# Kernel tuning notes

Measured on AMD Instinct MI355X. Metric: run time of the kernel, lower is better.

## Reference

```python
import jax, jax.numpy as jnp
import numpy as np

N_NODES = 100000
N_EDGES = 1600000
IN_DIM = 256
OUT_DIM = 128


def setup_inputs() -> dict:
    key = jax.random.key(0)
    k1, k2, k3, k4, k5 = jax.random.split(key, 5)
    x = jax.random.normal(k1, (N_NODES, IN_DIM), dtype=jnp.float32)
    W = jax.random.normal(k2, (OUT_DIM, IN_DIM), dtype=jnp.float32) * (1.0 / np.sqrt(IN_DIM))
    edge_row = jax.random.randint(k3, (N_EDGES,), 0, N_NODES, dtype=jnp.int32)
    edge_col = jax.random.randint(k4, (N_EDGES,), 0, N_NODES, dtype=jnp.int32)
    # normalized adjacency values (positive, like D^-1/2 A D^-1/2 entries)
    edge_val = jax.random.uniform(k5, (N_EDGES,), dtype=jnp.float32)
    return {"x": x, "W": W, "edge_row": edge_row, "edge_col": edge_col, "edge_val": edge_val}


def reference(x, W, edge_row, edge_col, edge_val):
    # h = x @ W.T  (Linear without bias), shape [N, out_dim]
    h = jnp.einsum('ni,oi->no', x, W)
    # SpMM: out[r] = sum_{e: row[e]==r} val[e] * h[col[e]]
    msgs = h[edge_col] * edge_val[:, None]           # [E, out_dim] irregular gather
    out = jax.ops.segment_sum(msgs, edge_row, num_segments=x.shape[0])
    return out
```

## Files before the change

kernel.cpp:

```cpp
#include <hip/hip_runtime.h>
#include <hip/hip_fp16.h>

#define N_NODES 100000
#define N_EDGES 1600000
#define IN_DIM  256
#define OUT_DIM 128

#define BROWS  256
#define NBKT   391
#define CAP    4608
#define CHUNK  8192
#define NBLK   196
#define DCAP   6144

#define BMT    32
#define NTILE  (N_NODES / BMT)
#define TPB    4
#define NGBLK  ((NTILE + TPB - 1) / TPB)

typedef __attribute__((ext_vector_type(8))) short short8;
typedef __attribute__((ext_vector_type(4))) float f32x4;
typedef __attribute__((ext_vector_type(2))) float f32x2;

__device__ __forceinline__ unsigned short f2bf(float f) {
    unsigned int u = __float_as_uint(f);
    u += 0x7FFFu + ((u >> 16) & 1u);
    return (unsigned short)(u >> 16);
}
__device__ __forceinline__ float bf2f(unsigned int u16) {
    return __uint_as_float(u16 << 16);
}

__device__ __forceinline__ short8 pack8(float4 a, float4 b) {
    short8 s;
    s[0] = (short)f2bf(a.x); s[1] = (short)f2bf(a.y);
    s[2] = (short)f2bf(a.z); s[3] = (short)f2bf(a.w);
    s[4] = (short)f2bf(b.x); s[5] = (short)f2bf(b.y);
    s[6] = (short)f2bf(b.z); s[7] = (short)f2bf(b.w);
    return s;
}

__global__ __launch_bounds__(256) void w_to_bf16(const float* __restrict__ W,
                                                 unsigned short* __restrict__ Wb,
                                                 int* __restrict__ bcnt) {
    int i = blockIdx.x * 256 + threadIdx.x;
    if (i < OUT_DIM * IN_DIM) Wb[i] = f2bf(W[i]);
    if (blockIdx.x == 0) {
        for (int b = threadIdx.x; b < NBKT; b += 256) bcnt[b] = 0;
    }
}

__global__ __launch_bounds__(512) void gemm_bin(const float* __restrict__ x,
                                                const unsigned short* __restrict__ Wb,
                                                unsigned short* __restrict__ hb,
                                                const int* __restrict__ erow,
                                                const int* __restrict__ ecol,
                                                const float* __restrict__ eval,
                                                int* __restrict__ bcnt,
                                                int2* __restrict__ gbuf) {
    __shared__ unsigned short xs[2 * BMT * 256];
    const int tid = threadIdx.x;

    if (blockIdx.x < NBLK) {
        int* h    = (int*)xs;
        int* gpos = h + NBKT;
        int* rcur = gpos + NBKT;
        for (int i = tid; i < NBKT; i += 512) { h[i] = 0; rcur[i] = 0; }
        __syncthreads();
        const int e0 = blockIdx.x * CHUNK;
        for (int i = tid; i < CHUNK; i += 512) {
            int e = e0 + i;
            if (e < N_EDGES) atomicAdd(&h[erow[e] >> 8], 1);
        }
        __syncthreads();
        for (int i = tid; i < NBKT; i += 512)
            gpos[i] = h[i] ? (i * CAP + atomicAdd(&bcnt[i], h[i])) : 0;
        __syncthreads();
        for (int i = tid; i < CHUNK; i += 512) {
            int e = e0 + i;
            if (e < N_EDGES) {
                int r = erow[e];
                int b = r >> 8;
                unsigned int vb  = __half_as_ushort(__float2half(eval[e]));
                unsigned int rec = (vb << 17) | (unsigned int)ecol[e];
                int pos = gpos[b] + atomicAdd(&rcur[b], 1);
                gbuf[pos] = make_int2((int)rec, r);
            }
        }
        return;
    }

    const int g    = blockIdx.x - NBLK;
    const int t0   = g * TPB;
    const int wid  = tid >> 6;
    const int lane = tid & 63;
    const int l15  = lane & 15;
    const int g8   = (lane >> 4) * 8;
    const int col  = wid * 16 + l15;
    const int sw   = (l15 & 7) << 4;
    char* lb = (char*)xs;

    const int srow = tid >> 4;
    const int ca   = (tid & 15) * 8;
    const int swr  = (srow & 7) << 4;
    const int wbA  = (srow * 512 + ca * 2) ^ swr;
    const int wbB  = (srow * 512 + (ca + 128) * 2) ^ swr;

    short8 bfr[8];
    const unsigned short* wrow = Wb + (size_t)col * IN_DIM + g8;
#pragma unroll
    for (int kk = 0; kk < 8; ++kk)
        bfr[kk] = *(const short8*)(wrow + kk * 32);

    {
        const int ti = t0;
        const int gr = (ti < NTILE) ? (ti * BMT + srow) : srow;
        const float4* sA = (const float4*)(x + (size_t)gr * IN_DIM + ca);
        const float4* sB = (const float4*)(x + (size_t)gr * IN_DIM + ca + 128);
        float4 f0 = sA[0], f1 = sA[1], f2 = sB[0], f3 = sB[1];
        *(short8*)(lb + wbA) = pack8(f0, f1);
        *(short8*)(lb + wbB) = pack8(f2, f3);
    }

#pragma unroll
    for (int i = 0; i < TPB; ++i) {
        float4 q0, q1, q2, q3;
        if (i + 1 < TPB) {
            const int ti = t0 + i + 1;
            const int gr = (ti < NTILE) ? (ti * BMT + srow) : srow;
            const float4* sA = (const float4*)(x + (size_t)gr * IN_DIM + ca);
            const float4* sB = (const float4*)(x + (size_t)gr * IN_DIM + ca + 128);
            q0 = sA[0]; q1 = sA[1]; q2 = sB[0]; q3 = sB[1];
        }
        __syncthreads();

        const int ti = t0 + i;
        const char* cb = lb + (i & 1) * (BMT * 512);
        short8 a0[8], a1[8];
#pragma unroll
        for (int kk = 0; kk < 8; ++kk) {
            a0[kk] = *(const short8*)(cb + ((l15 * 512 + (kk * 32 + g8) * 2) ^ sw));
            a1[kk] = *(const short8*)(cb + (((l15 + 16) * 512 + (kk * 32 + g8) * 2) ^ sw));
        }
        f32x4 acc0 = {0.f, 0.f, 0.f, 0.f}, acc1 = {0.f, 0.f, 0.f, 0.f};
#pragma unroll
        for (int kk = 0; kk < 8; ++kk) {
            acc0 = __builtin_amdgcn_mfma_f32_16x16x32_bf16(a0[kk], bfr[kk], acc0, 0, 0, 0);
            acc1 = __builtin_amdgcn_mfma_f32_16x16x32_bf16(a1[kk], bfr[kk], acc1, 0, 0, 0);
        }
        if (ti < NTILE) {
            const int rb0 = ti * BMT + (lane >> 4) * 4;
            const int rb1 = rb0 + 16;
#pragma unroll
            for (int q = 0; q < 4; ++q) {
                hb[(size_t)(rb0 + q) * OUT_DIM + col] = f2bf(acc0[q]);
                hb[(size_t)(rb1 + q) * OUT_DIM + col] = f2bf(acc1[q]);
            }
        }

        if (i + 1 < TPB) {
            char* wbuf = lb + ((i + 1) & 1) * (BMT * 512);
            *(short8*)(wbuf + wbA) = pack8(q0, q1);
            *(short8*)(wbuf + wbB) = pack8(q2, q3);
        }
    }
}

__global__ __launch_bounds__(256) void sort_bucket(const int2* __restrict__ gbuf,
                                                   const int* __restrict__ bcnt,
                                                   unsigned int* __restrict__ gcsr,
                                                   int* __restrict__ offs,
                                                   int* __restrict__ bend) {
    __shared__ int rh[BROWS], rc[BROWS], tmp[256];
    __shared__ unsigned int lout[DCAP];
    const int b    = blockIdx.x;
    const int base = b * CAP;
    const int cnt  = bcnt[b];
    const int r0   = b * BROWS;
    const int t    = threadIdx.x;

    rh[t] = 0;
    __syncthreads();
    for (int i = t; i < cnt; i += 256)
        atomicAdd(&rh[gbuf[base + i].y - r0], 1);
    __syncthreads();

    int v = rh[t];
    tmp[t] = v;
    __syncthreads();
    for (int d = 1; d < 256; d <<= 1) {
        int a = (t >= d) ? tmp[t - d] : 0;
        __syncthreads();
        tmp[t] += a;
        __syncthreads();
    }
    int ex = tmp[t] - v;
    rc[t] = ex;
    offs[r0 + t] = base + ex;
    if (t == 0) bend[b] = base + cnt;
    __syncthreads();

    if (cnt <= DCAP) {
        for (int i = t; i < cnt; i += 256) {
            int2 rr = gbuf[base + i];
            int p = atomicAdd(&rc[rr.y - r0], 1);
            lout[p] = (unsigned int)rr.x;
        }
        __syncthreads();
        for (int i = t; i < cnt; i += 256)
            gcsr[base + i] = lout[i];
    } else {
        for (int i = t; i < cnt; i += 256) {
            int2 rr = gbuf[base + i];
            int p = atomicAdd(&rc[rr.y - r0], 1);
            gcsr[base + p] = (unsigned int)rr.x;
        }
    }
}

__global__ __launch_bounds__(256) void spmm_gather(const unsigned short* __restrict__ hb,
                                                   const int* __restrict__ offs,
                                                   const int* __restrict__ bend,
                                                   const unsigned int* __restrict__ ccv,
                                                   float* __restrict__ out) {
    const int lane = threadIdx.x & 63;
    const int half = lane >> 5;
    const int li   = lane & 31;
    const int r    = blockIdx.x * 8 + (threadIdx.x >> 6) * 2 + half;

    const int js = offs[r];
    const int je = ((r & (BROWS - 1)) == (BROWS - 1)) ? bend[r >> 8] : offs[r + 1];

    f32x2 accA = {0.f, 0.f}, accB = {0.f, 0.f};
    for (int j = js; __any(j < je); j += 8) {
        unsigned int e[8];
        uint2 p[8];
#pragma unroll
        for (int q = 0; q < 8; ++q) {
            int jj = j + q;
            e[q] = ccv[jj < je ? jj : 0];
        }
#pragma unroll
        for (int q = 0; q < 8; ++q)
            p[q] = *(const uint2*)(hb + (size_t)(e[q] & 0x1FFFFu) * OUT_DIM + li * 4);
#pragma unroll
        for (int q = 0; q < 8; ++q) {
            float v = (j + q < je)
                    ? __half2float(__ushort_as_half((unsigned short)(e[q] >> 17)))
                    : 0.f;
            f32x2 vv  = {v, v};
            f32x2 h01 = { __uint_as_float(p[q].x << 16),
                          __uint_as_float(p[q].x & 0xFFFF0000u) };
            f32x2 h23 = { __uint_as_float(p[q].y << 16),
                          __uint_as_float(p[q].y & 0xFFFF0000u) };
            accA = __builtin_elementwise_fma(vv, h01, accA);
            accB = __builtin_elementwise_fma(vv, h23, accB);
        }
    }
    float4 o = {accA.x, accA.y, accB.x, accB.y};
    *(float4*)(out + (size_t)r * OUT_DIM + li * 4) = o;
}

__global__ __launch_bounds__(512) void gemm_plain(const float* __restrict__ x,
                                                  const float* __restrict__ W,
                                                  unsigned short* __restrict__ hb) {
    __shared__ unsigned short xs[2 * BMT * 256];
    const int tid = threadIdx.x;
    const int m0  = blockIdx.x * (2 * BMT);
    char* lb = (char*)xs;
    {
        const int row = tid >> 3;
        const int cs  = (tid & 7) * 32;
        const int gr  = m0 + row;
        if (gr < N_NODES) {
            const float4* src = (const float4*)(x + (size_t)gr * IN_DIM + cs);
#pragma unroll
            for (int i = 0; i < 4; ++i) {
                float4 a = src[2 * i], b = src[2 * i + 1];
                int byt = (row * 512 + (cs + 8 * i) * 2) ^ ((row & 7) << 4);
                *(short8*)(lb + byt) = pack8(a, b);
            }
        } else {
            short8 z = {0, 0, 0, 0, 0, 0, 0, 0};
#pragma unroll
            for (int i = 0; i < 4; ++i) {
                int byt = (row * 512 + (cs + 8 * i) * 2) ^ ((row & 7) << 4);
                *(short8*)(lb + byt) = z;
            }
        }
    }
    __syncthreads();
    const int wid  = tid >> 6;
    const int lane = tid & 63;
    const int l15  = lane & 15;
    const int g8   = (lane >> 4) * 8;
    short8 bfr[8];
    const float* wrowf = W + (size_t)(wid * 16 + l15) * IN_DIM + g8;
#pragma unroll
    for (int kk = 0; kk < 8; ++kk) {
        float4 wa = *(const float4*)(wrowf + kk * 32);
        float4 wb = *(const float4*)(wrowf + kk * 32 + 4);
        bfr[kk] = pack8(wa, wb);
    }
    const int col = wid * 16 + l15;
    const int sw  = (l15 & 7) << 4;
    const char* lbc = (const char*)xs;
#pragma unroll
    for (int rp = 0; rp < 2; ++rp) {
        const int r0 = rp * 32 + l15;
        const int r1 = r0 + 16;
        short8 a0[8], a1[8];
#pragma unroll
        for (int kk = 0; kk < 8; ++kk) {
            a0[kk] = *(const short8*)(lbc + ((r0 * 512 + (kk * 32 + g8) * 2) ^ sw));
            a1[kk] = *(const short8*)(lbc + ((r1 * 512 + (kk * 32 + g8) * 2) ^ sw));
        }
        f32x4 acc0 = {0.f, 0.f, 0.f, 0.f}, acc1 = {0.f, 0.f, 0.f, 0.f};
#pragma unroll
        for (int kk = 0; kk < 8; ++kk) {
            acc0 = __builtin_amdgcn_mfma_f32_16x16x32_bf16(a0[kk], bfr[kk], acc0, 0, 0, 0);
            acc1 = __builtin_amdgcn_mfma_f32_16x16x32_bf16(a1[kk], bfr[kk], acc1, 0, 0, 0);
        }
        const int rb0 = m0 + rp * 32 + (lane >> 4) * 4;
        const int rb1 = rb0 + 16;
#pragma unroll
        for (int i = 0; i < 4; ++i) {
            if (rb0 + i < N_NODES) hb[(size_t)(rb0 + i) * OUT_DIM + col] = f2bf(acc0[i]);
            if (rb1 + i < N_NODES) hb[(size_t)(rb1 + i) * OUT_DIM + col] = f2bf(acc1[i]);
        }
    }
}

__global__ __launch_bounds__(256) void spmm_scatter(const unsigned short* __restrict__ hb,
                                                    const int* __restrict__ erow,
                                                    const int* __restrict__ ecol,
                                                    const float* __restrict__ eval,
                                                    float* __restrict__ out) {
    const int lane = threadIdx.x & 63;
    const int eloc = threadIdx.x >> 6;
    const int stride = gridDim.x * 4;
    for (int e = blockIdx.x * 4 + eloc; e < N_EDGES; e += stride) {
        const int r = erow[e];
        const int c = ecol[e];
        const float v = eval[e];
        unsigned int p = *(const unsigned int*)(hb + (size_t)c * OUT_DIM + lane * 2);
        float* o = out + (size_t)r * OUT_DIM + lane * 2;
        unsafeAtomicAdd(o + 0, v * bf2f(p & 0xFFFFu));
        unsafeAtomicAdd(o + 1, v * bf2f(p >> 16));
    }
}

extern "C" void kernel_launch(void* const* d_in, const int* in_sizes, int n_in,
                              void* d_out, int out_size, void* d_ws, size_t ws_size,
                              hipStream_t stream) {
    const float* x    = (const float*)d_in[0];
    const float* W    = (const float*)d_in[1];
    const int*   erow = (const int*)d_in[2];
    const int*   ecol = (const int*)d_in[3];
    const float* eval = (const float*)d_in[4];
    float*       out  = (float*)d_out;

    const size_t H_ELEMS = (size_t)N_NODES * OUT_DIM;
    unsigned short* hb    = (unsigned short*)d_ws;
    int2*           gbuf  = (int2*)(hb + H_ELEMS);
    unsigned int*   gcsr  = (unsigned int*)(gbuf + (size_t)NBKT * CAP);
    int*            offs  = (int*)(gcsr + (size_t)NBKT * CAP);
    int*            bend  = offs + NBKT * BROWS + 8;
    int*            bcnt  = bend + NBKT;
    unsigned short* Wb    = (unsigned short*)(bcnt + NBKT + 8);
    const size_t need = ((char*)(Wb + OUT_DIM * IN_DIM)) - (char*)d_ws;

    if (ws_size >= need) {
        w_to_bf16<<<(OUT_DIM * IN_DIM + 255) / 256, 256, 0, stream>>>(W, Wb, bcnt);
        gemm_bin<<<NBLK + NGBLK, 512, 0, stream>>>(x, Wb, hb, erow, ecol, eval, bcnt, gbuf);
        sort_bucket<<<NBKT, 256, 0, stream>>>(gbuf, bcnt, gcsr, offs, bend);
        spmm_gather<<<N_NODES / 8, 256, 0, stream>>>(hb, offs, bend, gcsr, out);
    } else {
        gemm_plain<<<(N_NODES + 2 * BMT - 1) / (2 * BMT), 512, 0, stream>>>(x, W, hb);
        hipMemsetAsync(d_out, 0, (size_t)out_size * sizeof(float), stream);
        spmm_scatter<<<8192, 256, 0, stream>>>(hb, erow, ecol, eval, out);
    }
}
```

Measured before the change: 119.0 us.

## Split x conversion into pre-swizzled bf16 pass and async-LDS GEMM kernel

Adds a kernel that converts x to bf16 in a pre-swizzled tile layout, running alongside the edge binning, then a separate GEMM that pulls tiles straight into LDS with global_load_lds double buffering. The goal is to take the fp32 load and convert work off the MFMA loop and overlap the tile loads with compute. The cost is an extra write and read of a bf16 copy of x (about 51 MB total) and one more kernel launch. The gcsr buffer now shares workspace with xswz, which is safe because xswz is dead by the time sort_bucket runs.

After: 146.0 us. +22.7%, slower.

```diff
diff --git a/kernel.cpp b/kernel.cpp
--- a/kernel.cpp
+++ b/kernel.cpp
@@ -17,6 +17,9 @@
 #define NTILE  (N_NODES / BMT)
 #define TPB    4
 #define NGBLK  ((NTILE + TPB - 1) / TPB)
+#define BUFSZ  (BMT * 512)
+#define TPC    8
+#define NCVT   ((NTILE + TPC - 1) / TPC)
 
 typedef __attribute__((ext_vector_type(8))) short short8;
 typedef __attribute__((ext_vector_type(4))) float f32x4;
@@ -30,7 +33,6 @@
 __device__ __forceinline__ float bf2f(unsigned int u16) {
     return __uint_as_float(u16 << 16);
 }
-
 __device__ __forceinline__ short8 pack8(float4 a, float4 b) {
     short8 s;
     s[0] = (short)f2bf(a.x); s[1] = (short)f2bf(a.y);
@@ -40,13 +42,143 @@
     return s;
 }
 
+__device__ __forceinline__ void gload16(const void* g, void* l) {
+    __builtin_amdgcn_global_load_lds(
+        (const __attribute__((address_space(1))) unsigned int*)g,
+        (__attribute__((address_space(3))) unsigned int*)l, 16, 0, 0);
+}
+
 __global__ __launch_bounds__(256) void w_to_bf16(const float* __restrict__ W,
                                                  unsigned short* __restrict__ Wb,
                                                  int* __restrict__ bcnt) {
     int i = blockIdx.x * 256 + threadIdx.x;
     if (i < OUT_DIM * IN_DIM) Wb[i] = f2bf(W[i]);
-    if (blockIdx.x == 0) {
+    if (blockIdx.x == 0)
         for (int b = threadIdx.x; b < NBKT; b += 256) bcnt[b] = 0;
+}
+
+__global__ __launch_bounds__(512) void cvt_bin(const float* __restrict__ x,
+                                               unsigned short* __restrict__ xswz,
+                                               const int* __restrict__ erow,
+                                               const int* __restrict__ ecol,
+                                               const float* __restrict__ eval,
+                                               int* __restrict__ bcnt,
+                                               int2* __restrict__ gbuf) {
+    __shared__ int shm[3 * NBKT];
+    const int tid = threadIdx.x;
+
+    if (blockIdx.x < NBLK) {
+        int* h    = shm;
+        int* gpos = h + NBKT;
+        int* rcur = gpos + NBKT;
+        for (int i = tid; i < NBKT; i += 512) { h[i] = 0; rcur[i] = 0; }
+        __syncthreads();
+        const int e0 = blockIdx.x * CHUNK;
+        for (int i = tid; i < CHUNK; i += 512) {
+            int e = e0 + i;
+            if (e < N_EDGES) atomicAdd(&h[erow[e] >> 8], 1);
+        }
+        __syncthreads();
+        for (int i = tid; i < NBKT; i += 512)
+            gpos[i] = h[i] ? (i * CAP + atomicAdd(&bcnt[i], h[i])) : 0;
+        __syncthreads();
+        for (int i = tid; i < CHUNK; i += 512) {
+            int e = e0 + i;
+            if (e < N_EDGES) {
+                int r = erow[e];
+                int b = r >> 8;
+                unsigned int vb  = __half_as_ushort(__float2half(eval[e]));
+                unsigned int rec = (vb << 17) | (unsigned int)ecol[e];
+                int pos = gpos[b] + atomicAdd(&rcur[b], 1);
+                gbuf[pos] = make_int2((int)rec, r);
+            }
+        }
+        return;
+    }
+
+    const int tb  = (blockIdx.x - NBLK) * TPC;
+    const int row = tid >> 4;
+    const int c0  = (tid & 15) * 16;
+    const int sb  = (row & 7) << 4;
+    const int o0  = (row * 512 + c0 * 2) ^ sb;
+    const int o1  = (row * 512 + (c0 + 8) * 2) ^ sb;
+#pragma unroll
+    for (int q = 0; q < TPC; ++q) {
+        const int ti = tb + q;
+        if (ti < NTILE) {
+            const float4* src = (const float4*)(x + (size_t)(ti * BMT + row) * IN_DIM + c0);
+            float4 f0 = src[0], f1 = src[1], f2 = src[2], f3 = src[3];
+            char* dst = (char*)xswz + (size_t)ti * 16384;
+            *(short8*)(dst + o0) = pack8(f0, f1);
+            *(short8*)(dst + o1) = pack8(f2, f3);
+        }
+    }
+}
+
+__global__ __launch_bounds__(512) void gemm_async(const unsigned short* __restrict__ xswz,
+                                                  const unsigned short* __restrict__ Wb,
+                                                  unsigned short* __restrict__ hb) {
+    __shared__ unsigned short xs[2 * BMT * 256];
+    const int tid  = threadIdx.x;
+    const int t0   = blockIdx.x * TPB;
+    const int wid  = tid >> 6;
+    const int lane = tid & 63;
+    const int l15  = lane & 15;
+    const int g8   = (lane >> 4) * 8;
+    const int col  = wid * 16 + l15;
+    const int sw   = (l15 & 7) << 4;
+    char* lb = (char*)xs;
+    const char* xb = (const char*)xswz;
+
+    short8 bfr[8];
+    const unsigned short* wrow = Wb + (size_t)col * IN_DIM + g8;
+#pragma unroll
+    for (int kk = 0; kk < 8; ++kk)
+        bfr[kk] = *(const short8*)(wrow + kk * 32);
+
+    {
+        const int ti = (t0 < NTILE) ? t0 : 0;
+        const char* g = xb + (size_t)ti * 16384 + wid * 2048 + lane * 16;
+        char* l = lb + wid * 2048;
+        gload16(g, l);
+        gload16(g + 1024, l + 1024);
+    }
+
+#pragma unroll
+    for (int i = 0; i < TPB; ++i) {
+        __syncthreads();
+
+        if (i + 1 < TPB) {
+            const int tn = (t0 + i + 1 < NTILE) ? (t0 + i + 1) : 0;
+            const char* g = xb + (size_t)tn * 16384 + wid * 2048 + lane * 16;
+            char* l = lb + ((i + 1) & 1) * BUFSZ + wid * 2048;
+            gload16(g, l);
+            gload16(g + 1024, l + 1024);
+        }
+
+        const int ti = t0 + i;
+        if (ti < NTILE) {
+            const char* cb = lb + (i & 1) * BUFSZ;
+            short8 a0[8], a1[8];
+#pragma unroll
+            for (int kk = 0; kk < 8; ++kk) {
+                a0[kk] = *(const short8*)(cb + ((l15 * 512 + (kk * 32 + g8) * 2) ^ sw));
+                a1[kk] = *(const short8*)(cb + (((l15 + 16) * 512 + (kk * 32 + g8) * 2) ^ sw));
+            }
+            f32x4 acc0 = {0.f, 0.f, 0.f, 0.f}, acc1 = {0.f, 0.f, 0.f, 0.f};
+#pragma unroll
+            for (int kk = 0; kk < 8; ++kk) {
+                acc0 = __builtin_amdgcn_mfma_f32_16x16x32_bf16(a0[kk], bfr[kk], acc0, 0, 0, 0);
+                acc1 = __builtin_amdgcn_mfma_f32_16x16x32_bf16(a1[kk], bfr[kk], acc1, 0, 0, 0);
+            }
+            const int rb0 = ti * BMT + (lane >> 4) * 4;
+            const int rb1 = rb0 + 16;
+#pragma unroll
+            for (int q = 0; q < 4; ++q) {
+                hb[(size_t)(rb0 + q) * OUT_DIM + col] = f2bf(acc0[q]);
+                hb[(size_t)(rb1 + q) * OUT_DIM + col] = f2bf(acc1[q]);
+            }
+        }
     }
 }
 
@@ -99,7 +231,6 @@
     const int col  = wid * 16 + l15;
     const int sw   = (l15 & 7) << 4;
     char* lb = (char*)xs;
-
     const int srow = tid >> 4;
     const int ca   = (tid & 15) * 8;
     const int swr  = (srow & 7) << 4;
@@ -135,7 +266,7 @@
         __syncthreads();
 
         const int ti = t0 + i;
-        const char* cb = lb + (i & 1) * (BMT * 512);
+        const char* cb = lb + (i & 1) * BUFSZ;
         short8 a0[8], a1[8];
 #pragma unroll
         for (int kk = 0; kk < 8; ++kk) {
@@ -157,9 +288,8 @@
                 hb[(size_t)(rb1 + q) * OUT_DIM + col] = f2bf(acc1[q]);
             }
         }
-
         if (i + 1 < TPB) {
-            char* wbuf = lb + ((i + 1) & 1) * (BMT * 512);
+            char* wbuf = lb + ((i + 1) & 1) * BUFSZ;
             *(short8*)(wbuf + wbA) = pack8(q0, q1);
             *(short8*)(wbuf + wbB) = pack8(q2, q3);
         }
@@ -363,14 +493,25 @@
     const size_t H_ELEMS = (size_t)N_NODES * OUT_DIM;
     unsigned short* hb    = (unsigned short*)d_ws;
     int2*           gbuf  = (int2*)(hb + H_ELEMS);
-    unsigned int*   gcsr  = (unsigned int*)(gbuf + (size_t)NBKT * CAP);
-    int*            offs  = (int*)(gcsr + (size_t)NBKT * CAP);
+    int*            offs  = (int*)(gbuf + (size_t)NBKT * CAP);
     int*            bend  = offs + NBKT * BROWS + 8;
     int*            bcnt  = bend + NBKT;
     unsigned short* Wb    = (unsigned short*)(bcnt + NBKT + 8);
-    const size_t need = ((char*)(Wb + OUT_DIM * IN_DIM)) - (char*)d_ws;
-
-    if (ws_size >= need) {
+    char*           zraw  = (char*)(Wb + OUT_DIM * IN_DIM);
+    char*           Z     = zraw + ((16 - ((size_t)zraw & 15)) & 15);
+    unsigned short* xswz  = (unsigned short*)Z;
+    unsigned int*   gcsr  = (unsigned int*)Z;
+
+    const size_t need_full = (Z + (size_t)NTILE * 16384) - (char*)d_ws;
+    const size_t need_r19  = (Z + (size_t)NBKT * CAP * 4) - (char*)d_ws;
+
+    if (ws_size >= need_full) {
+        w_to_bf16<<<(OUT_DIM * IN_DIM + 255) / 256, 256, 0, stream>>>(W, Wb, bcnt);
+        cvt_bin<<<NBLK + NCVT, 512, 0, stream>>>(x, xswz, erow, ecol, eval, bcnt, gbuf);
+        gemm_async<<<NGBLK, 512, 0, stream>>>(xswz, Wb, hb);
+        sort_bucket<<<NBKT, 256, 0, stream>>>(gbuf, bcnt, gcsr, offs, bend);
+        spmm_gather<<<N_NODES / 8, 256, 0, stream>>>(hb, offs, bend, gcsr, out);
+    } else if (ws_size >= need_r19) {
         w_to_bf16<<<(OUT_DIM * IN_DIM + 255) / 256, 256, 0, stream>>>(W, Wb, bcnt);
         gemm_bin<<<NBLK + NGBLK, 512, 0, stream>>>(x, Wb, hb, erow, ecol, eval, bcnt, gbuf);
         sort_bucket<<<NBKT, 256, 0, stream>>>(gbuf, bcnt, gcsr, offs, bend);
```
